# Optimization experiments

Measured on AMD Instinct MI355X. Metric: run time of the kernel, lower is better.

## Reference

```python
import jax, jax.numpy as jnp
import numpy as np
import math

NUM_HEADS = 8
HEAD_DIM = 16  # hidden_features 128 / 8 heads
SCALE = 1.0 / math.sqrt(HEAD_DIM)


def setup_inputs() -> dict:
    key = jax.random.key(0)
    ks = jax.random.split(key, 9)
    N, E, F = 50000, 640000, 128
    node_h = jax.random.normal(ks[0], (N, F), jnp.float32)
    edge_h = jax.random.normal(ks[1], (E, F), jnp.float32)
    # distances kept strictly positive so distance**lambda (and its grad) is well-defined
    distance = jax.random.uniform(ks[2], (E, 1), jnp.float32, minval=0.1, maxval=1.0)
    src = jax.random.randint(ks[3], (E,), 0, N, jnp.int32)
    dst = jax.random.randint(ks[4], (E,), 0, N, jnp.int32)

    def lin(k):
        kw, kb = jax.random.split(k)
        W = jax.random.normal(kw, (F, F), jnp.float32) / math.sqrt(F)
        b = jax.random.normal(kb, (F,), jnp.float32) * 0.02
        return W, b

    Wq, bq = lin(ks[5])
    Wk, bk = lin(ks[6])
    Wv, bv = lin(ks[7])
    Wo, bo = lin(ks[8])
    lam = jnp.array(1.0, jnp.float32)  # attenuation_lambda (clamp in original is a no-op)
    return dict(node_h=node_h, edge_h=edge_h, distance=distance,
                Wq=Wq, bq=bq, Wk=Wk, bk=bk, Wv=Wv, bv=bv, Wo=Wo, bo=bo,
                lam=lam, src=src, dst=dst)


def _segment_softmax(logits, seg, num):
    # softmax over edges sharing the same destination node (DGL mailbox dim=1)
    m = jax.ops.segment_max(logits, seg, num_segments=num)
    m = jax.lax.stop_gradient(jnp.where(jnp.isfinite(m), m, 0.0))
    e = jnp.exp(logits - m[seg])
    den = jax.ops.segment_sum(e, seg, num_segments=num)
    den = jnp.where(den == 0, 1.0, den)  # guard zero in-degree nodes
    return e / den[seg]


def reference(node_h, edge_h, distance, Wq, bq, Wk, bk, Wv, bv, Wo, bo, lam, src, dst):
    N = node_h.shape[0]
    q = (node_h @ Wq.T + bq).reshape(N, NUM_HEADS, HEAD_DIM)
    k = (edge_h @ Wk.T + bk).reshape(-1, NUM_HEADS, HEAD_DIM)
    v = (node_h @ Wv.T + bv).reshape(N, NUM_HEADS, HEAD_DIM)
    qs, qd = q[src], q[dst]                      # [E, H, d] gathers
    in_m = jnp.sum(qs * k, axis=-1)              # [E, H]
    out_m = jnp.sum(qd * k, axis=-1)             # [E, H]
    diag_m = jnp.sum(qs * qd, axis=-1)           # [E, H]
    att = jnp.power(distance, lam)               # [E, 1] power-law attenuation
    score = (_segment_softmax(in_m * SCALE, dst, N)
             + _segment_softmax(out_m * SCALE, dst, N)
             + _segment_softmax(diag_m * SCALE, dst, N)) * att  # [E, H]
    # message value is edges.dst['v'] (as in the original), scatter-sum to dst
    h = jax.ops.segment_sum(score[..., None] * v[dst], dst, num_segments=N)
    h = h.reshape(N, NUM_HEADS * HEAD_DIM)
    out = h @ Wo.T + bo
    return jax.nn.leaky_relu(out, negative_slope=0.1)  # dropout is identity in eval
```

## Files before the change

kernel.cpp:

```cpp
#include <hip/hip_runtime.h>
#include <math.h>

#define H 8
#define FD 128
#define SCALE 0.25f

typedef __attribute__((ext_vector_type(8))) short bf16x8;
typedef __attribute__((ext_vector_type(4))) float f32x4;

__device__ __forceinline__ unsigned short bf_rne(float f) {
    unsigned u = __float_as_uint(f);
    u += 0x7FFFu + ((u >> 16) & 1u);
    return (unsigned short)(u >> 16);
}
__device__ __forceinline__ float bf_to_f(unsigned short s) {
    return __uint_as_float(((unsigned)s) << 16);
}
__device__ __forceinline__ bf16x8 cvt8(const float* __restrict__ p) {
    float4 a = *(const float4*)p;
    float4 b = *(const float4*)(p + 4);
    bf16x8 r;
    r[0] = bf_rne(a.x); r[1] = bf_rne(a.y); r[2] = bf_rne(a.z); r[3] = bf_rne(a.w);
    r[4] = bf_rne(b.x); r[5] = bf_rne(b.y); r[6] = bf_rne(b.z); r[7] = bf_rne(b.w);
    return r;
}

__global__ __launch_bounds__(256) void prep_kernel(
    const float* __restrict__ Wq, const float* __restrict__ Wk,
    const float* __restrict__ Wv, const float* __restrict__ Wo,
    unsigned short* __restrict__ oq, unsigned short* __restrict__ ok,
    unsigned short* __restrict__ ov, unsigned short* __restrict__ oo) {
    int i = blockIdx.x * 256 + threadIdx.x;
    const float* src[4] = {Wq, Wk, Wv, Wo};
    unsigned short* dstp[4] = {oq, ok, ov, oo};
#pragma unroll
    for (int m = 0; m < 4; ++m) {
        float4 w = ((const float4*)src[m])[i];
        ushort4 p = make_ushort4(bf_rne(w.x), bf_rne(w.y), bf_rne(w.z), bf_rne(w.w));
        *(ushort4*)(dstp[m] + i * 4) = p;
    }
}

__global__ __launch_bounds__(256) void qv_kernel(
    const float* __restrict__ X, const unsigned short* __restrict__ Wqb,
    const unsigned short* __restrict__ Wvb, const float* __restrict__ bq,
    const float* __restrict__ bv, unsigned short* __restrict__ qb,
    float* __restrict__ v, int Nrows) {
    const int t = threadIdx.x;
    const int lane = t & 63, wid = t >> 6;
    const int lm = lane & 15, lq = lane >> 4;
    const int r0 = blockIdx.x * 64 + wid * 16;

    bf16x8 a[4];
#pragma unroll
    for (int s = 0; s < 4; ++s) {
        int r = r0 + lm;
        if (r >= Nrows) r = Nrows - 1;
        a[s] = cvt8(X + (size_t)r * FD + s * 32 + lq * 8);
    }
#pragma unroll
    for (int g = 0; g < 2; ++g) {
        const unsigned short* Wb = g ? Wvb : Wqb;
        const float* bias = g ? bv : bq;
        f32x4 acc[8];
#pragma unroll
        for (int nt = 0; nt < 8; ++nt) {
            float b = bias[nt * 16 + lm];
            acc[nt][0] = b; acc[nt][1] = b; acc[nt][2] = b; acc[nt][3] = b;
        }
#pragma unroll
        for (int s = 0; s < 4; ++s)
#pragma unroll
            for (int nt = 0; nt < 8; ++nt) {
                bf16x8 bf = *(const bf16x8*)(Wb + (nt * 16 + lm) * FD + s * 32 + lq * 8);
                acc[nt] = __builtin_amdgcn_mfma_f32_16x16x32_bf16(
                    a[s], bf, acc[nt], 0, 0, 0);
            }
#pragma unroll
        for (int nt = 0; nt < 8; ++nt)
#pragma unroll
            for (int r = 0; r < 4; ++r) {
                int row = r0 + lq * 4 + r;
                if (row >= Nrows) continue;
                int col = nt * 16 + lm;
                if (g == 0)
                    qb[(size_t)row * FD + col] = bf_rne(acc[nt][r]);
                else
                    v[(size_t)row * FD + col] = acc[nt][r];
            }
    }
}

__global__ __launch_bounds__(256) void edge_kernel(
    const float* __restrict__ eh, const unsigned short* __restrict__ Wkb,
    const float* __restrict__ bk, const unsigned short* __restrict__ qb,
    const int* __restrict__ src, const int* __restrict__ dst,
    const float* __restrict__ distance, const float* __restrict__ lam,
    float* __restrict__ den1, float* __restrict__ den2,
    float* __restrict__ den3, float* __restrict__ sc1,
    float* __restrict__ sc2, float* __restrict__ sc3, int E) {
    __shared__ unsigned short lK[64 * 128];
    const int t = threadIdx.x;
    const int e0 = blockIdx.x * 64;
    const int lane = t & 63, wid = t >> 6;
    const int lm = lane & 15, lq = lane >> 4;
    const int wm = wid * 16;

    bf16x8 a[4];
#pragma unroll
    for (int s = 0; s < 4; ++s) {
        int e = e0 + wm + lm;
        if (e >= E) e = E - 1;
        a[s] = cvt8(eh + (size_t)e * FD + s * 32 + lq * 8);
    }
    f32x4 acc[8];
#pragma unroll
    for (int nt = 0; nt < 8; ++nt) {
        float b = bk[nt * 16 + lm];
        acc[nt][0] = b; acc[nt][1] = b; acc[nt][2] = b; acc[nt][3] = b;
    }
#pragma unroll
    for (int s = 0; s < 4; ++s)
#pragma unroll
        for (int nt = 0; nt < 8; ++nt) {
            bf16x8 bf = *(const bf16x8*)(Wkb + (nt * 16 + lm) * FD + s * 32 + lq * 8);
            acc[nt] = __builtin_amdgcn_mfma_f32_16x16x32_bf16(
                a[s], bf, acc[nt], 0, 0, 0);
        }
#pragma unroll
    for (int nt = 0; nt < 8; ++nt)
#pragma unroll
        for (int r = 0; r < 4; ++r) {
            int m = wm + lq * 4 + r;
            int n = nt * 16 + lm;
            int swb = (n >> 3) ^ (m & 7);
            lK[m * 128 + swb * 8 + (n & 7)] = bf_rne(acc[nt][r]);
        }
    __syncthreads();

    const float lamv = lam[0];
#pragma unroll
    for (int i = 0; i < 2; ++i) {
        int p = i * 256 + t;
        int el = p >> 3, h = p & 7;
        int e = e0 + el;
        if (e >= E) continue;
        int si = src[e], di = dst[e];
        const unsigned short* qsp = qb + (size_t)si * FD + h * 16;
        const unsigned short* qdp = qb + (size_t)di * FD + h * 16;
        bf16x8 qs0 = *(const bf16x8*)qsp;
        bf16x8 qs1 = *(const bf16x8*)(qsp + 8);
        bf16x8 qd0 = *(const bf16x8*)qdp;
        bf16x8 qd1 = *(const bf16x8*)(qdp + 8);
        int swb0 = (2 * h) ^ (el & 7), swb1 = (2 * h + 1) ^ (el & 7);
        bf16x8 k0 = *(const bf16x8*)(lK + el * 128 + swb0 * 8);
        bf16x8 k1 = *(const bf16x8*)(lK + el * 128 + swb1 * 8);
        float pin = 0.f, pot = 0.f, pdg = 0.f;
#pragma unroll
        for (int j = 0; j < 8; ++j) {
            float qsf = bf_to_f((unsigned short)qs0[j]);
            float qdf = bf_to_f((unsigned short)qd0[j]);
            float kf = bf_to_f((unsigned short)k0[j]);
            pin += qsf * kf; pot += qdf * kf; pdg += qsf * qdf;
        }
#pragma unroll
        for (int j = 0; j < 8; ++j) {
            float qsf = bf_to_f((unsigned short)qs1[j]);
            float qdf = bf_to_f((unsigned short)qd1[j]);
            float kf = bf_to_f((unsigned short)k1[j]);
            pin += qsf * kf; pot += qdf * kf; pdg += qsf * qdf;
        }
        float att = __expf(lamv * __logf(distance[e]));
        float e1 = __expf(pin * SCALE);
        float e2 = __expf(pot * SCALE);
        float e3 = __expf(pdg * SCALE);
        int nb = di * H + h;
        atomicAdd(den1 + nb, e1); atomicAdd(sc1 + nb, e1 * att);
        atomicAdd(den2 + nb, e2); atomicAdd(sc2 + nb, e2 * att);
        atomicAdd(den3 + nb, e3); atomicAdd(sc3 + nb, e3 * att);
    }
}

__global__ __launch_bounds__(256) void combine_kernel(
    const float* __restrict__ den1, const float* __restrict__ den2,
    const float* __restrict__ den3, const float* __restrict__ sc1,
    const float* __restrict__ sc2, const float* __restrict__ sc3,
    float* __restrict__ ssum, int NH) {
    int i = blockIdx.x * 256 + threadIdx.x;
    if (i >= NH) return;
    float r = 0.f;
    float d1 = den1[i]; if (d1 != 0.f) r += sc1[i] / d1;
    float d2 = den2[i]; if (d2 != 0.f) r += sc2[i] / d2;
    float d3 = den3[i]; if (d3 != 0.f) r += sc3[i] / d3;
    ssum[i] = r;
}

__global__ __launch_bounds__(256) void out_kernel(
    const float* __restrict__ v, const float* __restrict__ ssum,
    const unsigned short* __restrict__ Wob, const float* __restrict__ bo,
    float* __restrict__ out, int Nrows) {
    const int t = threadIdx.x;
    const int lane = t & 63, wid = t >> 6;
    const int lm = lane & 15, lq = lane >> 4;
    const int r0 = blockIdx.x * 64 + wid * 16;

    bf16x8 a[4];
#pragma unroll
    for (int s = 0; s < 4; ++s) {
        int r = r0 + lm;
        if (r >= Nrows) r = Nrows - 1;
        int k0 = s * 32 + lq * 8;
        float sc = ssum[r * H + (k0 >> 4)];
        const float* p = v + (size_t)r * FD + k0;
        float4 x = *(const float4*)p;
        float4 y = *(const float4*)(p + 4);
        bf16x8 f;
        f[0] = bf_rne(x.x * sc); f[1] = bf_rne(x.y * sc);
        f[2] = bf_rne(x.z * sc); f[3] = bf_rne(x.w * sc);
        f[4] = bf_rne(y.x * sc); f[5] = bf_rne(y.y * sc);
        f[6] = bf_rne(y.z * sc); f[7] = bf_rne(y.w * sc);
        a[s] = f;
    }
    f32x4 acc[8];
#pragma unroll
    for (int nt = 0; nt < 8; ++nt) {
        float b = bo[nt * 16 + lm];
        acc[nt][0] = b; acc[nt][1] = b; acc[nt][2] = b; acc[nt][3] = b;
    }
#pragma unroll
    for (int s = 0; s < 4; ++s)
#pragma unroll
        for (int nt = 0; nt < 8; ++nt) {
            bf16x8 bf = *(const bf16x8*)(Wob + (nt * 16 + lm) * FD + s * 32 + lq * 8);
            acc[nt] = __builtin_amdgcn_mfma_f32_16x16x32_bf16(
                a[s], bf, acc[nt], 0, 0, 0);
        }
#pragma unroll
    for (int nt = 0; nt < 8; ++nt)
#pragma unroll
        for (int r = 0; r < 4; ++r) {
            int row = r0 + lq * 4 + r;
            if (row >= Nrows) continue;
            int col = nt * 16 + lm;
            float x = acc[nt][r];
            out[(size_t)row * FD + col] = x > 0.f ? x : 0.1f * x;
        }
}

extern "C" void kernel_launch(void* const* d_in, const int* in_sizes, int n_in,
                              void* d_out, int out_size, void* d_ws,
                              size_t ws_size, hipStream_t stream) {
    (void)n_in; (void)out_size; (void)ws_size;
    const float* node_h   = (const float*)d_in[0];
    const float* edge_h   = (const float*)d_in[1];
    const float* distance = (const float*)d_in[2];
    const float* Wq = (const float*)d_in[3];
    const float* bq = (const float*)d_in[4];
    const float* Wk = (const float*)d_in[5];
    const float* bk = (const float*)d_in[6];
    const float* Wv = (const float*)d_in[7];
    const float* bv = (const float*)d_in[8];
    const float* Wo = (const float*)d_in[9];
    const float* bo = (const float*)d_in[10];
    const float* lam = (const float*)d_in[11];
    const int* src = (const int*)d_in[12];
    const int* dst = (const int*)d_in[13];

    int N = in_sizes[0] / FD;
    int E = in_sizes[1] / FD;
    int NH = N * H;

    char* ws = (char*)d_ws;
    unsigned short* Wqb = (unsigned short*)ws; ws += FD * FD * 2;
    unsigned short* Wkb = (unsigned short*)ws; ws += FD * FD * 2;
    unsigned short* Wvb = (unsigned short*)ws; ws += FD * FD * 2;
    unsigned short* Wob = (unsigned short*)ws; ws += FD * FD * 2;
    unsigned short* qb  = (unsigned short*)ws; ws += (size_t)N * FD * 2;
    float* v    = (float*)ws; ws += (size_t)N * FD * 4;
    char* zero_base = ws;
    float* den1 = (float*)ws; ws += (size_t)NH * 4;
    float* den2 = (float*)ws; ws += (size_t)NH * 4;
    float* den3 = (float*)ws; ws += (size_t)NH * 4;
    float* sc1  = (float*)ws; ws += (size_t)NH * 4;
    float* sc2  = (float*)ws; ws += (size_t)NH * 4;
    float* sc3  = (float*)ws; ws += (size_t)NH * 4;
    float* ssum = (float*)ws; ws += (size_t)NH * 4;

    hipMemsetAsync(zero_base, 0, (size_t)6 * NH * 4, stream);

    prep_kernel<<<16, 256, 0, stream>>>(Wq, Wk, Wv, Wo, Wqb, Wkb, Wvb, Wob);

    int nb = (N + 63) / 64;
    qv_kernel<<<nb, 256, 0, stream>>>(node_h, Wqb, Wvb, bq, bv, qb, v, N);

    int ebl = (E + 63) / 64;
    edge_kernel<<<ebl, 256, 0, stream>>>(edge_h, Wkb, bk, qb, src, dst,
                                         distance, lam,
                                         den1, den2, den3, sc1, sc2, sc3, E);

    combine_kernel<<<(NH + 255) / 256, 256, 0, stream>>>(
        den1, den2, den3, sc1, sc2, sc3, ssum, NH);

    out_kernel<<<nb, 256, 0, stream>>>(v, ssum, Wob, bo, (float*)d_out, N);
}
```

Baseline: 725.1 us.

## Replace atomic edge scatter with CSR-sorted segmented attention per destination

```diff
diff --git a/kernel.cpp b/kernel.cpp
--- a/kernel.cpp
+++ b/kernel.cpp
@@ -89,6 +89,166 @@
                     v[(size_t)row * FD + col] = acc[nt][r];
             }
     }
+}
+
+__global__ __launch_bounds__(256) void hist_kernel(
+    const int* __restrict__ dst, int* __restrict__ cnt, int E) {
+    int i = blockIdx.x * 256 + threadIdx.x;
+    if (i < E) atomicAdd(cnt + dst[i], 1);
+}
+
+__global__ __launch_bounds__(256) void scan1_kernel(
+    const int* __restrict__ cnt, int* __restrict__ offs,
+    int* __restrict__ bsum, int N) {
+    __shared__ int sd[256];
+    int t = threadIdx.x, i = blockIdx.x * 256 + t;
+    int x = (i < N) ? cnt[i] : 0;
+    int v = x;
+    sd[t] = v; __syncthreads();
+#pragma unroll
+    for (int off = 1; off < 256; off <<= 1) {
+        int y = (t >= off) ? sd[t - off] : 0;
+        __syncthreads();
+        v += y; sd[t] = v; __syncthreads();
+    }
+    if (i < N) offs[i] = v - x;
+    if (t == 255) bsum[blockIdx.x] = v;
+}
+
+__global__ __launch_bounds__(256) void scan2_kernel(int* __restrict__ bsum, int NB) {
+    __shared__ int sd[256];
+    int t = threadIdx.x;
+    int x = (t < NB) ? bsum[t] : 0;
+    int v = x;
+    sd[t] = v; __syncthreads();
+#pragma unroll
+    for (int off = 1; off < 256; off <<= 1) {
+        int y = (t >= off) ? sd[t - off] : 0;
+        __syncthreads();
+        v += y; sd[t] = v; __syncthreads();
+    }
+    if (t < NB) bsum[t] = v - x;
+}
+
+__global__ __launch_bounds__(256) void scan3_kernel(
+    int* __restrict__ offs, int* __restrict__ cursor,
+    const int* __restrict__ bsum, int N, int E) {
+    int i = blockIdx.x * 256 + threadIdx.x;
+    if (i < N) {
+        int o = offs[i] + bsum[blockIdx.x];
+        offs[i] = o;
+        cursor[i] = o;
+    }
+    if (i == 0) offs[N] = E;
+}
+
+__global__ __launch_bounds__(256) void scatter_kernel(
+    const int* __restrict__ src, const int* __restrict__ dst,
+    const float* __restrict__ distance, const float* __restrict__ lam,
+    int* __restrict__ cursor, int* __restrict__ rank,
+    int* __restrict__ srcs_s, float* __restrict__ att_s, int E) {
+    int i = blockIdx.x * 256 + threadIdx.x;
+    if (i >= E) return;
+    int d = dst[i];
+    int r = atomicAdd(cursor + d, 1);
+    rank[i] = r;
+    srcs_s[r] = src[i];
+    att_s[r] = __expf(lam[0] * __logf(distance[i]));
+}
+
+__global__ __launch_bounds__(256) void kproj_sorted_kernel(
+    const float* __restrict__ X, const unsigned short* __restrict__ Wkb,
+    const float* __restrict__ bk, const int* __restrict__ rank,
+    unsigned short* __restrict__ kb, int E) {
+    const int t = threadIdx.x;
+    const int lane = t & 63, wid = t >> 6;
+    const int lm = lane & 15, lq = lane >> 4;
+    const int r0 = blockIdx.x * 64 + wid * 16;
+
+    bf16x8 a[4];
+#pragma unroll
+    for (int s = 0; s < 4; ++s) {
+        int r = r0 + lm;
+        if (r >= E) r = E - 1;
+        a[s] = cvt8(X + (size_t)r * FD + s * 32 + lq * 8);
+    }
+    f32x4 acc[8];
+#pragma unroll
+    for (int nt = 0; nt < 8; ++nt) {
+        float b = bk[nt * 16 + lm];
+        acc[nt][0] = b; acc[nt][1] = b; acc[nt][2] = b; acc[nt][3] = b;
+    }
+#pragma unroll
+    for (int s = 0; s < 4; ++s)
+#pragma unroll
+        for (int nt = 0; nt < 8; ++nt) {
+            bf16x8 bf = *(const bf16x8*)(Wkb + (nt * 16 + lm) * FD + s * 32 + lq * 8);
+            acc[nt] = __builtin_amdgcn_mfma_f32_16x16x32_bf16(
+                a[s], bf, acc[nt], 0, 0, 0);
+        }
+#pragma unroll
+    for (int r = 0; r < 4; ++r) {
+        int e = r0 + lq * 4 + r;
+        if (e >= E) continue;
+        int rk = rank[e];
+        unsigned short* dstrow = kb + (size_t)rk * FD + lm;
+#pragma unroll
+        for (int nt = 0; nt < 8; ++nt)
+            dstrow[nt * 16] = bf_rne(acc[nt][r]);
+    }
+}
+
+__global__ __launch_bounds__(256) void seg_attn_kernel(
+    const unsigned short* __restrict__ kb, const unsigned short* __restrict__ qb,
+    const int* __restrict__ offs, const int* __restrict__ srcs_s,
+    const float* __restrict__ att_s, float* __restrict__ ssum, int NH) {
+    int i = blockIdx.x * 256 + threadIdx.x;
+    if (i >= NH) return;
+    int n = i >> 3, h = i & 7;
+    int s0 = offs[n], s1 = offs[n + 1];
+
+    const unsigned short* qdp = qb + (size_t)n * FD + h * 16;
+    bf16x8 qd0 = *(const bf16x8*)qdp;
+    bf16x8 qd1 = *(const bf16x8*)(qdp + 8);
+
+    float den1 = 0.f, den2 = 0.f, den3 = 0.f;
+    float a1 = 0.f, a2 = 0.f, a3 = 0.f;
+    for (int j = s0; j < s1; ++j) {
+        const unsigned short* kp = kb + (size_t)j * FD + h * 16;
+        bf16x8 k0 = *(const bf16x8*)kp;
+        bf16x8 k1 = *(const bf16x8*)(kp + 8);
+        int s = srcs_s[j];
+        const unsigned short* qsp = qb + (size_t)s * FD + h * 16;
+        bf16x8 qs0 = *(const bf16x8*)qsp;
+        bf16x8 qs1 = *(const bf16x8*)(qsp + 8);
+        float att = att_s[j];
+        float pin = 0.f, pot = 0.f, pdg = 0.f;
+#pragma unroll
+        for (int q = 0; q < 8; ++q) {
+            float qsf = bf_to_f((unsigned short)qs0[q]);
+            float qdf = bf_to_f((unsigned short)qd0[q]);
+            float kf  = bf_to_f((unsigned short)k0[q]);
+            pin += qsf * kf; pot += qdf * kf; pdg += qsf * qdf;
+        }
+#pragma unroll
+        for (int q = 0; q < 8; ++q) {
+            float qsf = bf_to_f((unsigned short)qs1[q]);
+            float qdf = bf_to_f((unsigned short)qd1[q]);
+            float kf  = bf_to_f((unsigned short)k1[q]);
+            pin += qsf * kf; pot += qdf * kf; pdg += qsf * qdf;
+        }
+        float e1 = __expf(pin * SCALE);
+        float e2 = __expf(pot * SCALE);
+        float e3 = __expf(pdg * SCALE);
+        den1 += e1; a1 += e1 * att;
+        den2 += e2; a2 += e2 * att;
+        den3 += e3; a3 += e3 * att;
+    }
+    float r = 0.f;
+    if (den1 != 0.f) r += a1 / den1;
+    if (den2 != 0.f) r += a2 / den2;
+    if (den3 != 0.f) r += a3 / den3;
+    ssum[i] = r;
 }
 
 __global__ __launch_bounds__(256) void edge_kernel(
@@ -250,7 +410,7 @@
 extern "C" void kernel_launch(void* const* d_in, const int* in_sizes, int n_in,
                               void* d_out, int out_size, void* d_ws,
                               size_t ws_size, hipStream_t stream) {
-    (void)n_in; (void)out_size; (void)ws_size;
+    (void)n_in; (void)out_size;
     const float* node_h   = (const float*)d_in[0];
     const float* edge_h   = (const float*)d_in[1];
     const float* distance = (const float*)d_in[2];
@@ -269,37 +429,74 @@
     int N = in_sizes[0] / FD;
     int E = in_sizes[1] / FD;
     int NH = N * H;
-
-    char* ws = (char*)d_ws;
-    unsigned short* Wqb = (unsigned short*)ws; ws += FD * FD * 2;
-    unsigned short* Wkb = (unsigned short*)ws; ws += FD * FD * 2;
-    unsigned short* Wvb = (unsigned short*)ws; ws += FD * FD * 2;
-    unsigned short* Wob = (unsigned short*)ws; ws += FD * FD * 2;
-    unsigned short* qb  = (unsigned short*)ws; ws += (size_t)N * FD * 2;
-    float* v    = (float*)ws; ws += (size_t)N * FD * 4;
-    char* zero_base = ws;
-    float* den1 = (float*)ws; ws += (size_t)NH * 4;
-    float* den2 = (float*)ws; ws += (size_t)NH * 4;
-    float* den3 = (float*)ws; ws += (size_t)NH * 4;
-    float* sc1  = (float*)ws; ws += (size_t)NH * 4;
-    float* sc2  = (float*)ws; ws += (size_t)NH * 4;
-    float* sc3  = (float*)ws; ws += (size_t)NH * 4;
-    float* ssum = (float*)ws; ws += (size_t)NH * 4;
-
-    hipMemsetAsync(zero_base, 0, (size_t)6 * NH * 4, stream);
+    int NB = (N + 255) / 256;
+
+    char* p = (char*)d_ws;
+    auto alloc = [&](size_t bytes) -> char* {
+        char* r = p;
+        p += (bytes + 255) & ~(size_t)255;
+        return r;
+    };
+    unsigned short* Wqb = (unsigned short*)alloc(FD * FD * 2);
+    unsigned short* Wkb = (unsigned short*)alloc(FD * FD * 2);
+    unsigned short* Wvb = (unsigned short*)alloc(FD * FD * 2);
+    unsigned short* Wob = (unsigned short*)alloc(FD * FD * 2);
+    unsigned short* qb  = (unsigned short*)alloc((size_t)N * FD * 2);
+    float* v    = (float*)alloc((size_t)N * FD * 4);
+    float* ssum = (float*)alloc((size_t)NH * 4);
+    char* branch_base = p;
+
+    int* cnt    = (int*)alloc((size_t)N * 4);
+    int* offs   = (int*)alloc((size_t)(N + 1) * 4);
+    int* cursor = (int*)alloc((size_t)N * 4);
+    int* bsum   = (int*)alloc((size_t)NB * 4);
+    int* rank   = (int*)alloc((size_t)E * 4);
+    int* srcs_s = (int*)alloc((size_t)E * 4);
+    float* att_s = (float*)alloc((size_t)E * 4);
+    unsigned short* kb = (unsigned short*)alloc((size_t)E * FD * 2);
+    size_t need_main = (size_t)(p - (char*)d_ws);
+
+    bool main_ok = (ws_size >= need_main) && (NB <= 256);
 
     prep_kernel<<<16, 256, 0, stream>>>(Wq, Wk, Wv, Wo, Wqb, Wkb, Wvb, Wob);
 
     int nb = (N + 63) / 64;
     qv_kernel<<<nb, 256, 0, stream>>>(node_h, Wqb, Wvb, bq, bv, qb, v, N);
 
-    int ebl = (E + 63) / 64;
-    edge_kernel<<<ebl, 256, 0, stream>>>(edge_h, Wkb, bk, qb, src, dst,
-                                         distance, lam,
-                                         den1, den2, den3, sc1, sc2, sc3, E);
-
-    combine_kernel<<<(NH + 255) / 256, 256, 0, stream>>>(
-        den1, den2, den3, sc1, sc2, sc3, ssum, NH);
+    if (main_ok) {
+        hipMemsetAsync(cnt, 0, (size_t)N * 4, stream);
+        int eb = (E + 255) / 256;
+        hist_kernel<<<eb, 256, 0, stream>>>(dst, cnt, E);
+        scan1_kernel<<<NB, 256, 0, stream>>>(cnt, offs, bsum, N);
+        scan2_kernel<<<1, 256, 0, stream>>>(bsum, NB);
+        scan3_kernel<<<NB, 256, 0, stream>>>(offs, cursor, bsum, N, E);
+        scatter_kernel<<<eb, 256, 0, stream>>>(src, dst, distance, lam,
+                                               cursor, rank, srcs_s, att_s, E);
+        kproj_sorted_kernel<<<(E + 63) / 64, 256, 0, stream>>>(
+            edge_h, Wkb, bk, rank, kb, E);
+        seg_attn_kernel<<<(NH + 255) / 256, 256, 0, stream>>>(
+            kb, qb, offs, srcs_s, att_s, ssum, NH);
+    } else {
+        char* q = branch_base;
+        auto alloc2 = [&](size_t bytes) -> char* {
+            char* r = q;
+            q += (bytes + 255) & ~(size_t)255;
+            return r;
+        };
+        float* den1 = (float*)alloc2((size_t)NH * 4);
+        float* den2 = (float*)alloc2((size_t)NH * 4);
+        float* den3 = (float*)alloc2((size_t)NH * 4);
+        float* sc1  = (float*)alloc2((size_t)NH * 4);
+        float* sc2  = (float*)alloc2((size_t)NH * 4);
+        float* sc3  = (float*)alloc2((size_t)NH * 4);
+        hipMemsetAsync(den1, 0, (size_t)(q - (char*)den1), stream);
+        int ebl = (E + 63) / 64;
+        edge_kernel<<<ebl, 256, 0, stream>>>(edge_h, Wkb, bk, qb, src, dst,
+                                             distance, lam,
+                                             den1, den2, den3, sc1, sc2, sc3, E);
+        combine_kernel<<<(NH + 255) / 256, 256, 0, stream>>>(
+            den1, den2, den3, sc1, sc2, sc3, ssum, NH);
+    }
 
     out_kernel<<<nb, 256, 0, stream>>>(v, ssum, Wob, bo, (float*)d_out, N);
 }
```

Result: slower. 822.6 us (+13.4%).
